# Kernel optimization log

Measured on AMD Instinct MI355X. Metric: run time of the kernel, lower is better.

The kernel has to match this reference:

```python
import jax, jax.numpy as jnp
import numpy as np

N, C, H, W = 8, 128, 56, 56
CO = C // 8  # 16


def setup_inputs() -> dict:
    key = jax.random.key(0)
    k1, k2, k3, k4 = jax.random.split(key, 4)
    x = jax.random.normal(k1, (N, C, H, W), dtype=jnp.float32)
    # p_3: Conv2d(c*35 -> c//8, 1x1). The unfold channel order is (c, kh=5, kw=7),
    # so the 1x1 conv over c*35 channels is exactly a dilated 5x7 conv with
    # weight [CO, C, 5, 7] and rhs_dilation (2, 3).
    w3 = jax.random.normal(k2, (CO, C, 5, 7), dtype=jnp.float32) * 0.02
    w4 = jax.random.normal(k3, (CO, CO), dtype=jnp.float32) * 0.1
    w5 = jax.random.normal(k4, (C, CO), dtype=jnp.float32) * 0.1
    return {"x": x, "w3": w3, "w4": w4, "w5": w5}


def reference(x, w3, w4, w5):
    # Fused equivalent of: unfold(5x1, dil 2, pad 4) -> unfold(1x7, dil 3, pad 9)
    # -> 1x1 conv (c*35 -> c//8). Padding (4,4)/(9,9) keeps 'same' spatial size.
    y = jax.lax.conv_general_dilated(
        x, w3,
        window_strides=(1, 1),
        padding=((4, 4), (9, 9)),
        rhs_dilation=(2, 3),
        dimension_numbers=("NCHW", "OIHW", "NCHW"),
    )  # [N, CO, H, W]
    y = jnp.einsum("oc,nchw->nohw", w4, y)  # p_4: 1x1 conv CO->CO
    y = jnp.einsum("oc,nchw->nohw", w5, y)  # p_5: 1x1 conv CO->C
    return y
```

## Files before the change

### kernel.cpp

```cpp
#include <hip/hip_runtime.h>

#define BN 8
#define BC 128
#define BH 56
#define BW 56
#define HW 3136
#define NTAP 35
#define WS_WC 71680
#define WS_XP (WS_WC + 4096)
#define XROW 2368
#define XPLANE (64 * XROW)

typedef unsigned short u16;
typedef unsigned int u32;
typedef __bf16 bf16x8 __attribute__((ext_vector_type(8)));
typedef float f32x4 __attribute__((ext_vector_type(4)));

__device__ __forceinline__ u16 f2b(float f) {
    unsigned u = __float_as_uint(f);
    return (u16)((u + 0x7FFFu + ((u >> 16) & 1u)) >> 16);
}
__device__ __forceinline__ u32 pack2(float a, float b) {
    return (u32)f2b(a) | ((u32)f2b(b) << 16);
}
__device__ __forceinline__ void dma16(const void* g, void* l) {
    __builtin_amdgcn_global_load_lds(
        (const __attribute__((address_space(1))) u32*)g,
        (__attribute__((address_space(3))) u32*)l, 16, 0, 0);
}

__global__ void prep_w(const float* __restrict__ w3, const float* __restrict__ w4,
                       const float* __restrict__ w5, u16* __restrict__ ws)
{
    int i = blockIdx.x * 256 + threadIdx.x;
    if (i < WS_WC) {
        int j = i & 7, lane = (i >> 3) & 63, r = i >> 9;
        int tap = r % NTAP, cc = r / NTAP;
        int q = lane >> 4, lm = lane & 15;
        ws[i] = f2b(w3[(lm * BC + cc * 32 + q * 8 + j) * NTAP + tap]);
    } else if (i < WS_WC + 4096) {
        int i2 = i - WS_WC;
        int j = i2 & 7, lane = (i2 >> 3) & 63, ot = i2 >> 9;
        int q = lane >> 4, lm = lane & 15, o = ot * 16 + lm, k = q * 8 + j;
        float s = 0.f;
        if (k < 16)
            for (int c = 0; c < 16; ++c) s += w5[o * 16 + c] * w4[c * 16 + k];
        ws[i] = f2b(s);
    }
}

__global__ __launch_bounds__(256) void prep_x(const float* __restrict__ x,
                                              u16* __restrict__ ws)
{
    __shared__ float ls[32][57];
    const int b = blockIdx.x;
    const int hp = b & 63, cc = (b >> 6) & 3, n = b >> 8;
    const int tid = threadIdx.x;
    u32* dst = (u32*)(ws + WS_XP + (size_t)((n * 4 + cc) * 64 + hp) * XROW);
    const int gr = hp - 4;

    if ((unsigned)gr >= BH) {
        for (int i = tid; i < XROW / 2; i += 256) dst[i] = 0u;
        return;
    }
    for (int i = tid; i < 32 * 14; i += 256) {
        int c = i / 14, w4 = i % 14;
        float4 v = *(const float4*)(x + ((size_t)(n * BC + cc * 32 + c) * BH + gr) * BW + 4 * w4);
        ls[c][4 * w4 + 0] = v.x;
        ls[c][4 * w4 + 1] = v.y;
        ls[c][4 * w4 + 2] = v.z;
        ls[c][4 * w4 + 3] = v.w;
    }
    __syncthreads();
    for (int i = tid; i < 74 * 16; i += 256) {
        int col = i >> 4, cp = i & 15;
        int gw = col - 9;
        u32 v = 0u;
        if ((unsigned)gw < BW) v = pack2(ls[2 * cp][gw], ls[2 * cp + 1][gw]);
        dst[col * 16 + cp] = v;
    }
}

__global__ __launch_bounds__(256) void conv_mfma(
    const u16* __restrict__ wsT, float* __restrict__ out)
{
    __shared__ __align__(16) u16 xs[5][74][32];
    __shared__ __align__(16) u16 wA[NTAP][64][8];
    __shared__ __align__(16) u16 y3T[64][40];

    const int n = blockIdx.x & 7, h = blockIdx.x >> 3;
    const int tid = threadIdx.x, lane = tid & 63, wv = tid >> 6;
    const int q = lane >> 4, lm = lane & 15, wpos = wv * 16 + lm;

    for (int i = tid; i < 512; i += 256) {
        int w = i >> 3, d = i & 7;
        ((u32*)&y3T[w][16])[d] = 0u;
    }

    f32x4 acc = {0.f, 0.f, 0.f, 0.f};
    char* xsf = (char*)&xs[0][0][0];
    char* wAf = (char*)&wA[0][0][0];

    for (int cc = 0; cc < 4; ++cc) {
        __syncthreads();

        const u16* xbase = wsT + WS_XP + (size_t)((n * 4 + cc) * 64 + h) * XROW;
        for (int k = wv; k < 24; k += 4) {
            int bb = k * 1024 + lane * 16;
            int r = bb / 4736;
            int off = bb - r * 4736;
            const u16* g = xbase + (size_t)(2 * r) * XROW + (off >> 1);
            if (k < 23 || lane < 8) dma16(g, xsf + bb);
        }
        const u16* wbase = wsT + (size_t)cc * NTAP * 512;
        for (int k = wv; k < NTAP; k += 4)
            dma16(wbase + (size_t)k * 512 + lane * 8, wAf + k * 1024 + lane * 16);

        __syncthreads();

        #pragma unroll
        for (int t = 0; t < NTAP; ++t) {
            const int kh = t / 7, kw = t % 7;
            bf16x8 a = *(const bf16x8*)&wA[t][lane][0];
            bf16x8 b = *(const bf16x8*)&xs[kh][wpos + 3 * kw][q * 8];
            acc = __builtin_amdgcn_mfma_f32_16x16x32_bf16(a, b, acc, 0, 0, 0);
        }
    }

    *(u32*)&y3T[wpos][q * 4]     = pack2(acc[0], acc[1]);
    *(u32*)&y3T[wpos][q * 4 + 2] = pack2(acc[2], acc[3]);
    __syncthreads();

    bf16x8 bfrag = *(const bf16x8*)&y3T[wpos][q * 8];
    const bool wok = (wpos < BW);
    #pragma unroll
    for (int ot = 0; ot < 8; ++ot) {
        bf16x8 afrag = *(const bf16x8*)(wsT + WS_WC + (size_t)(ot * 64 + lane) * 8);
        f32x4 c2 = {0.f, 0.f, 0.f, 0.f};
        c2 = __builtin_amdgcn_mfma_f32_16x16x32_bf16(afrag, bfrag, c2, 0, 0, 0);
        if (wok) {
            int o = ot * 16 + q * 4;
            float* po = out + ((size_t)(n * BC + o) * BH + h) * BW + wpos;
            po[0]      = c2[0];
            po[HW]     = c2[1];
            po[2 * HW] = c2[2];
            po[3 * HW] = c2[3];
        }
    }
}

extern "C" void kernel_launch(void* const* d_in, const int* in_sizes, int n_in,
                              void* d_out, int out_size, void* d_ws, size_t ws_size,
                              hipStream_t stream)
{
    (void)in_sizes; (void)n_in; (void)out_size; (void)ws_size;
    const float* x  = (const float*)d_in[0];
    const float* w3 = (const float*)d_in[1];
    const float* w4 = (const float*)d_in[2];
    const float* w5 = (const float*)d_in[3];
    u16* ws = (u16*)d_ws;

    prep_w<<<(WS_WC + 4096) / 256, 256, 0, stream>>>(w3, w4, w5, ws);
    prep_x<<<BN * 4 * 64, 256, 0, stream>>>(x, ws);
    conv_mfma<<<BN * BH, 256, 0, stream>>>(ws, (float*)d_out);
}
```

Baseline: 92.77 us.

## Merge weight and input prep kernels; load conv weights directly from global

The separate weight-prep and input-prep kernels become a single launch, with block index ranges choosing the role, so one kernel launch and one inter-kernel gap go away. The conv kernel no longer stages per-chunk weights into LDS through DMA. Each lane reads its bf16x8 weight fragment straight from global memory, where it is expected to hit cache, which shrinks LDS use and lets launch_bounds request four blocks per CU. The trade-off is 35 global loads per chunk inside the MFMA loop instead of LDS reads, which may expose latency.

```diff
diff --git a/kernel.cpp b/kernel.cpp
--- a/kernel.cpp
+++ b/kernel.cpp
@@ -9,7 +9,6 @@
 #define WS_WC 71680
 #define WS_XP (WS_WC + 4096)
 #define XROW 2368
-#define XPLANE (64 * XROW)
 
 typedef unsigned short u16;
 typedef unsigned int u32;
@@ -29,33 +28,35 @@
         (__attribute__((address_space(3))) u32*)l, 16, 0, 0);
 }
 
-__global__ void prep_w(const float* __restrict__ w3, const float* __restrict__ w4,
-                       const float* __restrict__ w5, u16* __restrict__ ws)
+__global__ __launch_bounds__(256) void prep_all(
+    const float* __restrict__ x, const float* __restrict__ w3,
+    const float* __restrict__ w4, const float* __restrict__ w5,
+    u16* __restrict__ ws)
 {
-    int i = blockIdx.x * 256 + threadIdx.x;
-    if (i < WS_WC) {
-        int j = i & 7, lane = (i >> 3) & 63, r = i >> 9;
-        int tap = r % NTAP, cc = r / NTAP;
-        int q = lane >> 4, lm = lane & 15;
-        ws[i] = f2b(w3[(lm * BC + cc * 32 + q * 8 + j) * NTAP + tap]);
-    } else if (i < WS_WC + 4096) {
-        int i2 = i - WS_WC;
-        int j = i2 & 7, lane = (i2 >> 3) & 63, ot = i2 >> 9;
-        int q = lane >> 4, lm = lane & 15, o = ot * 16 + lm, k = q * 8 + j;
-        float s = 0.f;
-        if (k < 16)
-            for (int c = 0; c < 16; ++c) s += w5[o * 16 + c] * w4[c * 16 + k];
-        ws[i] = f2b(s);
+    const int b = blockIdx.x;
+    const int tid = threadIdx.x;
+
+    if (b >= 2048) {
+        int i = (b - 2048) * 256 + tid;
+        if (i < WS_WC) {
+            int j = i & 7, lane = (i >> 3) & 63, r = i >> 9;
+            int tap = r % NTAP, cc = r / NTAP;
+            int q = lane >> 4, lm = lane & 15;
+            ws[i] = f2b(w3[(lm * BC + cc * 32 + q * 8 + j) * NTAP + tap]);
+        } else if (i < WS_WC + 4096) {
+            int i2 = i - WS_WC;
+            int j = i2 & 7, lane = (i2 >> 3) & 63, ot = i2 >> 9;
+            int q = lane >> 4, lm = lane & 15, o = ot * 16 + lm, k = q * 8 + j;
+            float s = 0.f;
+            if (k < 16)
+                for (int c = 0; c < 16; ++c) s += w5[o * 16 + c] * w4[c * 16 + k];
+            ws[i] = f2b(s);
+        }
+        return;
     }
-}
 
-__global__ __launch_bounds__(256) void prep_x(const float* __restrict__ x,
-                                              u16* __restrict__ ws)
-{
     __shared__ float ls[32][57];
-    const int b = blockIdx.x;
     const int hp = b & 63, cc = (b >> 6) & 3, n = b >> 8;
-    const int tid = threadIdx.x;
     u32* dst = (u32*)(ws + WS_XP + (size_t)((n * 4 + cc) * 64 + hp) * XROW);
     const int gr = hp - 4;
 
@@ -64,12 +65,12 @@
         return;
     }
     for (int i = tid; i < 32 * 14; i += 256) {
-        int c = i / 14, w4 = i % 14;
-        float4 v = *(const float4*)(x + ((size_t)(n * BC + cc * 32 + c) * BH + gr) * BW + 4 * w4);
-        ls[c][4 * w4 + 0] = v.x;
-        ls[c][4 * w4 + 1] = v.y;
-        ls[c][4 * w4 + 2] = v.z;
-        ls[c][4 * w4 + 3] = v.w;
+        int c = i / 14, w4i = i % 14;
+        float4 v = *(const float4*)(x + ((size_t)(n * BC + cc * 32 + c) * BH + gr) * BW + 4 * w4i);
+        ls[c][4 * w4i + 0] = v.x;
+        ls[c][4 * w4i + 1] = v.y;
+        ls[c][4 * w4i + 2] = v.z;
+        ls[c][4 * w4i + 3] = v.w;
     }
     __syncthreads();
     for (int i = tid; i < 74 * 16; i += 256) {
@@ -81,25 +82,22 @@
     }
 }
 
-__global__ __launch_bounds__(256) void conv_mfma(
+__global__ __launch_bounds__(256, 4) void conv_mfma(
     const u16* __restrict__ wsT, float* __restrict__ out)
 {
     __shared__ __align__(16) u16 xs[5][74][32];
-    __shared__ __align__(16) u16 wA[NTAP][64][8];
     __shared__ __align__(16) u16 y3T[64][40];
 
     const int n = blockIdx.x & 7, h = blockIdx.x >> 3;
     const int tid = threadIdx.x, lane = tid & 63, wv = tid >> 6;
     const int q = lane >> 4, lm = lane & 15, wpos = wv * 16 + lm;
 
-    for (int i = tid; i < 512; i += 256) {
-        int w = i >> 3, d = i & 7;
-        ((u32*)&y3T[w][16])[d] = 0u;
-    }
+    for (int i = tid; i < 512; i += 256)
+        ((u32*)&y3T[i >> 3][16])[i & 7] = 0u;
 
     f32x4 acc = {0.f, 0.f, 0.f, 0.f};
     char* xsf = (char*)&xs[0][0][0];
-    char* wAf = (char*)&wA[0][0][0];
+    const u16* ap = wsT + (size_t)lane * 8;
 
     for (int cc = 0; cc < 4; ++cc) {
         __syncthreads();
@@ -109,19 +107,16 @@
             int bb = k * 1024 + lane * 16;
             int r = bb / 4736;
             int off = bb - r * 4736;
-            const u16* g = xbase + (size_t)(2 * r) * XROW + (off >> 1);
-            if (k < 23 || lane < 8) dma16(g, xsf + bb);
+            if (k < 23 || lane < 8)
+                dma16(xbase + (size_t)(2 * r) * XROW + (off >> 1), xsf + bb);
         }
-        const u16* wbase = wsT + (size_t)cc * NTAP * 512;
-        for (int k = wv; k < NTAP; k += 4)
-            dma16(wbase + (size_t)k * 512 + lane * 8, wAf + k * 1024 + lane * 16);
-
         __syncthreads();
 
+        const u16* at = ap + (size_t)cc * NTAP * 512;
         #pragma unroll
         for (int t = 0; t < NTAP; ++t) {
             const int kh = t / 7, kw = t % 7;
-            bf16x8 a = *(const bf16x8*)&wA[t][lane][0];
+            bf16x8 a = *(const bf16x8*)(at + t * 512);
             bf16x8 b = *(const bf16x8*)&xs[kh][wpos + 3 * kw][q * 8];
             acc = __builtin_amdgcn_mfma_f32_16x16x32_bf16(a, b, acc, 0, 0, 0);
         }
@@ -160,7 +155,6 @@
     const float* w5 = (const float*)d_in[3];
     u16* ws = (u16*)d_ws;
 
-    prep_w<<<(WS_WC + 4096) / 256, 256, 0, stream>>>(w3, w4, w5, ws);
-    prep_x<<<BN * 4 * 64, 256, 0, stream>>>(x, ws);
+    prep_all<<<2048 + 296, 256, 0, stream>>>(x, w3, w4, w5, ws);
     conv_mfma<<<BN * BH, 256, 0, stream>>>(ws, (float*)d_out);
 }
```

After: 91.89 us. About the same (-0.9%).
